# Kernel tuning notes

Measured on AMD Instinct MI355X. Metric: run time of the kernel, lower is better.

Reference implementation:

```python
import jax, jax.numpy as jnp
import numpy as np

INPUT_SIZE = 3072
CORE_SIZE = 1024
OUTPUT_SIZE = 100
BATCH = 8192


def _ri(key, shape, lo, hi):
    # small-range int8 values (torch rand*scale cast to int8)
    return jax.random.randint(key, shape, lo, hi, dtype=jnp.int32).astype(jnp.int8)


def setup_inputs() -> dict:
    key = jax.random.key(0)
    ks = jax.random.split(key, 14)
    return {
        # learned int8 weights (nonzero after EQI.apply updates)
        "W_itoc": _ri(ks[0], (INPUT_SIZE, CORE_SIZE), -3, 4),
        "W_itoc_b": _ri(ks[1], (CORE_SIZE,), -3, 4),
        "W_ctoc": _ri(ks[2], (CORE_SIZE, CORE_SIZE), -3, 4),
        "W_ctoc_b": _ri(ks[3], (CORE_SIZE,), -3, 4),
        "W_ctoo": _ri(ks[4], (CORE_SIZE, OUTPUT_SIZE), -3, 4),
        "W_ctoo_b": _ri(ks[5], (OUTPUT_SIZE,), -3, 4),
        # epsilon perturbations: EPSILON_SCALE=2 -> values in {-1,0,1}
        "e_itoc": _ri(ks[6], (INPUT_SIZE, CORE_SIZE), -2, 2),
        "e_itoc_b": _ri(ks[7], (CORE_SIZE,), -2, 2),
        "e_ctoc": _ri(ks[8], (CORE_SIZE, CORE_SIZE), -2, 2),
        "e_ctoc_b": _ri(ks[9], (CORE_SIZE,), -2, 2),
        "e_ctoo": _ri(ks[10], (CORE_SIZE, OUTPUT_SIZE), -2, 2),
        "e_ctoo_b": _ri(ks[11], (OUTPUT_SIZE,), -2, 2),
        # forward activations
        "inputs": _ri(ks[12], (BATCH, INPUT_SIZE), -4, 5),
        "hiddens": _ri(ks[13], (BATCH, CORE_SIZE), -4, 5),
    }


def _addmm_i8(x, w, b):
    # int8 addmm with wraparound semantics: accumulate in int32, cast back
    # to int8 (truncation == mod-256, matching torch int8 arithmetic).
    acc = jnp.matmul(x.astype(jnp.int32), w.astype(jnp.int32)) + b.astype(jnp.int32)
    return acc.astype(jnp.int8)


def reference(W_itoc, W_itoc_b, W_ctoc, W_ctoc_b, W_ctoo, W_ctoo_b,
              e_itoc, e_itoc_b, e_ctoc, e_ctoc_b, e_ctoo, e_ctoo_b,
              inputs, hiddens):
    # layer 1: inputs -> core (weight = W + epsilon, elementwise int8 add)
    i2c = _addmm_i8(inputs, W_itoc + e_itoc, W_itoc_b + e_itoc_b)      # [B, CORE]
    # layer 2: (hiddens + projected inputs) -> core
    h2 = _addmm_i8(hiddens + i2c, W_ctoc + e_ctoc, W_ctoc_b + e_ctoc_b)  # [B, CORE]
    # layer 3: core -> output
    out = _addmm_i8(h2, W_ctoo + e_ctoo, W_ctoo_b + e_ctoo_b)          # [B, OUT]
    return (h2, out)
```

## Files before the change

### kernel.cpp

```cpp
#include <hip/hip_runtime.h>

typedef int v4i  __attribute__((ext_vector_type(4)));
typedef int v16i __attribute__((ext_vector_type(16)));

__device__ __forceinline__ int pack4i(int a, int b, int c, int d) {
  return (a & 255) | ((b & 255) << 8) | ((c & 255) << 16) | ((d & 255) << 24);
}
__device__ __forceinline__ int badd4(int a, int b) {
  return ((a & 0x7f7f7f7f) + (b & 0x7f7f7f7f)) ^ ((a ^ b) & 0x80808080);
}

__device__ void pack_tile(const int* __restrict__ W, const int* __restrict__ E,
                          char* __restrict__ Bt, int K, int N,
                          int nx, int ky, char* lin) {
  const int t = threadIdx.x;
  const int n0 = nx * 64, k0 = ky * 256;
  {
    const int c  = t & 15;
    const int kq = t >> 4;
    const int ng = n0 + c * 4;
    #pragma unroll 4
    for (int s = 0; s < 16; ++s) {
      const int k = s * 16 + kq;
      const long grow = (long)(k0 + k) * N;
      int a0, a1, a2, a3;
      if (ng + 3 < N) {
        int4 wv = *(const int4*)(W + grow + ng);
        int4 ev = *(const int4*)(E + grow + ng);
        a0 = wv.x + ev.x; a1 = wv.y + ev.y; a2 = wv.z + ev.z; a3 = wv.w + ev.w;
      } else {
        a0 = (ng + 0 < N) ? W[grow + ng + 0] + E[grow + ng + 0] : 0;
        a1 = (ng + 1 < N) ? W[grow + ng + 1] + E[grow + ng + 1] : 0;
        a2 = (ng + 2 < N) ? W[grow + ng + 2] + E[grow + ng + 2] : 0;
        a3 = (ng + 3 < N) ? W[grow + ng + 3] + E[grow + ng + 3] : 0;
      }
      *(int*)(lin + k * 68 + c * 4) = pack4i(a0, a1, a2, a3);
    }
  }
  __syncthreads();
  {
    const int n = t & 63, kq = t >> 6;
    char* dst = Bt + (long)(n0 + n) * K + k0 + (kq << 6);
    int outv[16];
    #pragma unroll
    for (int g = 0; g < 16; ++g) {
      const int k = (kq << 6) + (g << 2);
      outv[g] = pack4i(lin[(k + 0) * 68 + n], lin[(k + 1) * 68 + n],
                       lin[(k + 2) * 68 + n], lin[(k + 3) * 68 + n]);
    }
    #pragma unroll
    for (int g = 0; g < 4; ++g)
      *(int4*)(dst + (g << 4)) =
          make_int4(outv[g * 4], outv[g * 4 + 1], outv[g * 4 + 2], outv[g * 4 + 3]);
  }
}

__global__ __launch_bounds__(256) void pack_weights_kernel(
    const int* W1, const int* E1, char* Bt1,
    const int* W2, const int* E2, char* Bt2,
    const int* W3, const int* E3, char* Bt3,
    const int* b1, const int* eb1, int* bs1,
    const int* b2, const int* eb2, int* bs2,
    const int* b3, const int* eb3, int* bs3) {
  __shared__ __align__(16) char smem[17408];
  const int bid = blockIdx.x;
  if (bid < 192) {
    pack_tile(W1, E1, Bt1, 3072, 1024, bid % 16, bid / 16, smem);
  } else if (bid < 256) {
    const int l = bid - 192;
    pack_tile(W2, E2, Bt2, 1024, 1024, l % 16, l / 16, smem);
  } else if (bid < 264) {
    const int l = bid - 256;
    pack_tile(W3, E3, Bt3, 1024, 100, l & 1, l >> 1, smem);
  } else {
    const int t = threadIdx.x;
    for (int i = t; i < 1024; i += 256) {
      bs1[i] = b1[i] + eb1[i];
      bs2[i] = b2[i] + eb2[i];
    }
    for (int i = t; i < 128; i += 256)
      bs3[i] = (i < 100) ? (b3[i] + eb3[i]) : 0;
  }
}

#define MFMA_I8(a, b, c) __builtin_amdgcn_mfma_i32_32x32x32_i8(a, b, c, 0, 0, 0)

__global__ __launch_bounds__(512, 2) void gemm1_kernel(
    const int* __restrict__ X, const char* __restrict__ Btg,
    const int* __restrict__ bsum, const int* __restrict__ H,
    char* __restrict__ A8out) {
  const int K = 3072;
  __shared__ __align__(16) char smem[61440];
  const int t = threadIdx.x;
  const int bid = blockIdx.x;
  const int mt = bid & 63, nt = bid >> 6;
  const long m0 = (long)mt << 7;
  const int n0 = nt << 8;

  const int lane = t & 63, w = t >> 6;
  const int lc = lane & 31, hg = lane >> 5;
  const int wm = w >> 2, wn = w & 3;

  v16i acc[2][2] = {};

  const int arow = t >> 2, aq = t & 3;
  const int* Xrow = X + (m0 + arow) * (long)K + aq * 16;
  const int aoff = arow * 80 + aq * 16;
  const int brow = t >> 1, bh = t & 1;
  const char* Brow = Btg + (long)(n0 + brow) * K + bh * 32;
  const int boff = 10240 + brow * 80 + bh * 32;

  const int aro = (wm * 64 + lc) * 80 + hg * 16;
  const int bro = 10240 + (wn * 64 + lc) * 80 + hg * 16;

  int4 xa0, xa1, xa2, xa3, xb0, xb1;
  int4 ya0, ya1, ya2, ya3, yb0, yb1;

#define G1_LOAD(p0,p1,p2,p3,p4,p5,kt) do {                        \
    const int kb_ = (kt) << 6;                                    \
    const int* p_ = Xrow + kb_;                                   \
    p0 = *(const int4*)(p_);      p1 = *(const int4*)(p_ + 4);    \
    p2 = *(const int4*)(p_ + 8);  p3 = *(const int4*)(p_ + 12);   \
    p4 = *(const int4*)(Brow + kb_);                              \
    p5 = *(const int4*)(Brow + kb_ + 16);                         \
  } while (0)
#define G1_STORE(p0,p1,p2,p3,p4,p5,stage) do {                    \
    char* base_ = smem + (stage) * 30720;                         \
    *(int4*)(base_ + aoff) = make_int4(                           \
        pack4i(p0.x,p0.y,p0.z,p0.w), pack4i(p1.x,p1.y,p1.z,p1.w), \
        pack4i(p2.x,p2.y,p2.z,p2.w), pack4i(p3.x,p3.y,p3.z,p3.w));\
    *(int4*)(base_ + boff)      = p4;                             \
    *(int4*)(base_ + boff + 16) = p5;                             \
  } while (0)

  auto MFMA_STEP = [&](int stage) {
    const char* base = smem + stage * 30720;
    #pragma unroll
    for (int ks = 0; ks < 2; ++ks) {
      v4i a0 = *(const v4i*)(base + aro + ks * 32);
      v4i a1 = *(const v4i*)(base + aro + 32 * 80 + ks * 32);
      v4i b0 = *(const v4i*)(base + bro + ks * 32);
      v4i b1 = *(const v4i*)(base + bro + 32 * 80 + ks * 32);
      acc[0][0] = MFMA_I8(a0, b0, acc[0][0]);
      acc[0][1] = MFMA_I8(a0, b1, acc[0][1]);
      acc[1][0] = MFMA_I8(a1, b0, acc[1][0]);
      acc[1][1] = MFMA_I8(a1, b1, acc[1][1]);
    }
  };

  const int KIT = K >> 6;
  G1_LOAD(xa0, xa1, xa2, xa3, xb0, xb1, 0);
  G1_LOAD(ya0, ya1, ya2, ya3, yb0, yb1, 1);
  G1_STORE(xa0, xa1, xa2, xa3, xb0, xb1, 0);
  __syncthreads();

  for (int kt = 0; kt < KIT; kt += 2) {
    if (kt + 2 < KIT) G1_LOAD(xa0, xa1, xa2, xa3, xb0, xb1, kt + 2);
    MFMA_STEP(0);
    G1_STORE(ya0, ya1, ya2, ya3, yb0, yb1, 1);
    __syncthreads();
    if (kt + 3 < KIT) G1_LOAD(ya0, ya1, ya2, ya3, yb0, yb1, kt + 3);
    MFMA_STEP(1);
    if (kt + 2 < KIT) {
      G1_STORE(xa0, xa1, xa2, xa3, xb0, xb1, 0);
      __syncthreads();
    }
  }

  __syncthreads();
  const int bsj0 = bsum[n0 + wn * 64 + lc];
  const int bsj1 = bsum[n0 + wn * 64 + 32 + lc];
  #pragma unroll
  for (int i = 0; i < 2; ++i) {
    #pragma unroll
    for (int j = 0; j < 2; ++j) {
      const int bsv = j ? bsj1 : bsj0;
      const int col = wn * 64 + j * 32 + lc;
      #pragma unroll
      for (int r = 0; r < 16; ++r) {
        const int row = wm * 64 + i * 32 + (hg << 2) + (r & 3) + ((r >> 2) << 3);
        smem[row * 272 + col] = (char)(acc[i][j][r] + bsv);
      }
    }
  }
  __syncthreads();
  const int erow = t >> 2, seg = t & 3;
  const char* src = smem + erow * 272 + seg * 64;
  const long gm = m0 + erow;
  const long gco = gm * 1024 + n0 + seg * 64;
  const int* hp = H + gco;
  #pragma unroll
  for (int g = 0; g < 4; ++g) {
    int4 s  = *(const int4*)(src + g * 16);
    int4 h0 = *(const int4*)(hp + g * 16);
    int4 h1 = *(const int4*)(hp + g * 16 + 4);
    int4 h2 = *(const int4*)(hp + g * 16 + 8);
    int4 h3 = *(const int4*)(hp + g * 16 + 12);
    s = make_int4(badd4(s.x, pack4i(h0.x, h0.y, h0.z, h0.w)),
                  badd4(s.y, pack4i(h1.x, h1.y, h1.z, h1.w)),
                  badd4(s.z, pack4i(h2.x, h2.y, h2.z, h2.w)),
                  badd4(s.w, pack4i(h3.x, h3.y, h3.z, h3.w)));
    *(int4*)(A8out + gco + g * 16) = s;
  }
}

__global__ __launch_bounds__(512, 2) void gemm2_kernel(
    const char* __restrict__ A, const char* __restrict__ Btg,
    const int* __restrict__ bsum, int* __restrict__ Iout) {
  const int K = 1024;
  __shared__ __align__(16) char smem[61440];
  const int t = threadIdx.x;
  const int bid = blockIdx.x;
  const int mt = bid & 63, nt = bid >> 6;
  const long m0 = (long)mt << 7;
  const int n0 = nt << 8;

  const int lane = t & 63, w = t >> 6;
  const int lc = lane & 31, hg = lane >> 5;
  const int wm = w >> 2, wn = w & 3;

  v16i acc[2][2] = {};

  const int arow = t >> 2, aq = t & 3;
  const char* Arow = A + (m0 + arow) * (long)K + aq * 16;
  const int aoff = arow * 80 + aq * 16;
  const int brow = t >> 1, bh = t & 1;
  const char* Brow = Btg + (long)(n0 + brow) * K + bh * 32;
  const int boff = 10240 + brow * 80 + bh * 32;

  const int aro = (wm * 64 + lc) * 80 + hg * 16;
  const int bro = 10240 + (wn * 64 + lc) * 80 + hg * 16;

  int4 xa0, xb0, xb1;
  int4 ya0, yb0, yb1;

#define G2_LOAD(p0,p4,p5,kt) do {                                 \
    const int kb_ = (kt) << 6;                                    \
    p0 = *(const int4*)(Arow + kb_);                              \
    p4 = *(const int4*)(Brow + kb_);                              \
    p5 = *(const int4*)(Brow + kb_ + 16);                         \
  } while (0)
#define G2_STORE(p0,p4,p5,stage) do {                             \
    char* base_ = smem + (stage) * 30720;                         \
    *(int4*)(base_ + aoff)      = p0;                             \
    *(int4*)(base_ + boff)      = p4;                             \
    *(int4*)(base_ + boff + 16) = p5;                             \
  } while (0)

  auto MFMA_STEP = [&](int stage) {
    const char* base = smem + stage * 30720;
    #pragma unroll
    for (int ks = 0; ks < 2; ++ks) {
      v4i a0 = *(const v4i*)(base + aro + ks * 32);
      v4i a1 = *(const v4i*)(base + aro + 32 * 80 + ks * 32);
      v4i b0 = *(const v4i*)(base + bro + ks * 32);
      v4i b1 = *(const v4i*)(base + bro + 32 * 80 + ks * 32);
      acc[0][0] = MFMA_I8(a0, b0, acc[0][0]);
      acc[0][1] = MFMA_I8(a0, b1, acc[0][1]);
      acc[1][0] = MFMA_I8(a1, b0, acc[1][0]);
      acc[1][1] = MFMA_I8(a1, b1, acc[1][1]);
    }
  };

  const int KIT = K >> 6;
  G2_LOAD(xa0, xb0, xb1, 0);
  G2_LOAD(ya0, yb0, yb1, 1);
  G2_STORE(xa0, xb0, xb1, 0);
  __syncthreads();

  for (int kt = 0; kt < KIT; kt += 2) {
    if (kt + 2 < KIT) G2_LOAD(xa0, xb0, xb1, kt + 2);
    MFMA_STEP(0);
    G2_STORE(ya0, yb0, yb1, 1);
    __syncthreads();
    if (kt + 3 < KIT) G2_LOAD(ya0, yb0, yb1, kt + 3);
    MFMA_STEP(1);
    if (kt + 2 < KIT) {
      G2_STORE(xa0, xb0, xb1, 0);
      __syncthreads();
    }
  }

  const int bsj0 = bsum[n0 + wn * 64 + lc];
  const int bsj1 = bsum[n0 + wn * 64 + 32 + lc];
  #pragma unroll
  for (int i = 0; i < 2; ++i) {
    #pragma unroll
    for (int j = 0; j < 2; ++j) {
      const int bsv = j ? bsj1 : bsj0;
      const int col = n0 + wn * 64 + j * 32 + lc;
      #pragma unroll
      for (int r = 0; r < 16; ++r) {
        const long row = m0 + wm * 64 + i * 32 + (hg << 2) + (r & 3) + ((r >> 2) << 3);
        Iout[row * 1024 + col] = (int)(signed char)(acc[i][j][r] + bsv);
      }
    }
  }
}

__global__ __launch_bounds__(256, 2) void gemm3_kernel(
    const int* __restrict__ h2, const char* __restrict__ Btg,
    const int* __restrict__ bsum, int* __restrict__ Iout) {
  __shared__ __align__(16) char smem[23040];
  const int t = threadIdx.x;
  const int m0 = blockIdx.x << 4;
  const int lane = t & 63, w = t >> 6;
  const int l16 = lane & 15, q = lane >> 4;
  v4i acc0 = {}, acc1 = {};

  const int am = t >> 4, ah = t & 15;
  const int* Arow = h2 + (long)(m0 + am) * 1024 + ah * 4;
  const int aoff = am * 80 + ah * 4;
  const int bm = t >> 1, bh = t & 1;
  const char* Brow = Btg + (long)bm * 1024 + bh * 32;
  const int boff = bm * 80 + bh * 32;

  const int abo  = l16 * 80 + q * 16;
  const int bbo0 = (w * 32 + l16) * 80 + q * 16;
  const int bbo1 = (w * 32 + 16 + l16) * 80 + q * 16;

  int4 ar, br0, br1;
  auto LOAD = [&](int kt) {
    const int kb = kt << 6;
    ar  = *(const int4*)(Arow + kb);
    br0 = *(const int4*)(Brow + kb);
    br1 = *(const int4*)(Brow + kb + 16);
  };
  auto STORE = [&](int stage) {
    char* base = smem + stage * 11520;
    *(int*)(base + aoff) = pack4i(ar.x, ar.y, ar.z, ar.w);
    *(int4*)(base + 1280 + boff)      = br0;
    *(int4*)(base + 1280 + boff + 16) = br1;
  };
  auto MFMA = [&](int stage) {
    const char* base = smem + stage * 11520;
    v4i a  = *(const v4i*)(base + abo);
    v4i b0 = *(const v4i*)(base + 1280 + bbo0);
    v4i b1 = *(const v4i*)(base + 1280 + bbo1);
    acc0 = __builtin_amdgcn_mfma_i32_16x16x64_i8(a, b0, acc0, 0, 0, 0);
    acc1 = __builtin_amdgcn_mfma_i32_16x16x64_i8(a, b1, acc1, 0, 0, 0);
  };

  LOAD(0); STORE(0); __syncthreads();
  for (int kt = 0; kt < 16; ++kt) {
    if (kt + 1 < 16) LOAD(kt + 1);
    MFMA(kt & 1);
    if (kt + 1 < 16) { STORE((kt + 1) & 1); __syncthreads(); }
  }

  const int c0 = w * 32 + l16;
  const int c1 = c0 + 16;
  if (c0 < 100) {
    const int b = bsum[c0];
    #pragma unroll
    for (int r = 0; r < 4; ++r)
      Iout[(long)(m0 + q * 4 + r) * 100 + c0] = (int)(signed char)(acc0[r] + b);
  }
  if (c1 < 100) {
    const int b = bsum[c1];
    #pragma unroll
    for (int r = 0; r < 4; ++r)
      Iout[(long)(m0 + q * 4 + r) * 100 + c1] = (int)(signed char)(acc1[r] + b);
  }
}

extern "C" void kernel_launch(void* const* d_in, const int* in_sizes, int n_in,
                              void* d_out, int out_size, void* d_ws, size_t ws_size,
                              hipStream_t stream) {
  (void)in_sizes; (void)n_in; (void)out_size; (void)ws_size;
  const int* W1  = (const int*)d_in[0];
  const int* b1  = (const int*)d_in[1];
  const int* W2  = (const int*)d_in[2];
  const int* b2  = (const int*)d_in[3];
  const int* W3  = (const int*)d_in[4];
  const int* b3  = (const int*)d_in[5];
  const int* E1  = (const int*)d_in[6];
  const int* eb1 = (const int*)d_in[7];
  const int* E2  = (const int*)d_in[8];
  const int* eb2 = (const int*)d_in[9];
  const int* E3  = (const int*)d_in[10];
  const int* eb3 = (const int*)d_in[11];
  const int* X   = (const int*)d_in[12];
  const int* H   = (const int*)d_in[13];
  int* out = (int*)d_out;

  char* ws  = (char*)d_ws;
  char* Bt1 = ws;
  char* Bt2 = Bt1 + 3145728;
  char* Bt3 = Bt2 + 1048576;
  int*  bs1 = (int*)(Bt3 + 131072);
  int*  bs2 = bs1 + 1024;
  int*  bs3 = bs2 + 1024;
  char* A2  = (char*)(bs3 + 128);

  pack_weights_kernel<<<dim3(265), dim3(256), 0, stream>>>(
      W1, E1, Bt1, W2, E2, Bt2, W3, E3, Bt3,
      b1, eb1, bs1, b2, eb2, bs2, b3, eb3, bs3);

  gemm1_kernel<<<dim3(256), dim3(512), 0, stream>>>(X, Bt1, bs1, H, A2);

  gemm2_kernel<<<dim3(256), dim3(512), 0, stream>>>(A2, Bt2, bs2, out);

  gemm3_kernel<<<dim3(512), dim3(256), 0, stream>>>(
      out, Bt3, bs3, out + 8388608);
}
```

Baseline: 310.6 us.

## Use async global-to-LDS loads with triple-buffered swizzled tiles in GEMM1/GEMM2

Rewrites the two big int8 GEMMs to use 128x128 tiles with 256 threads, doubling the grid. B (and A in gemm2) tiles move via direct global-to-LDS async loads into an XOR-swizzled, unpadded layout with a three-stage ring, and explicit vmcnt waits replace full syncs. MFMA blocks run at raised wave priority. The aim is to cut register staging, LDS bank conflicts and barrier stalls, at the cost of smaller tiles with less reuse per block and fragile hand-managed wait counts.

```diff
diff --git a/kernel.cpp b/kernel.cpp
--- a/kernel.cpp
+++ b/kernel.cpp
@@ -9,6 +9,17 @@
 __device__ __forceinline__ int badd4(int a, int b) {
   return ((a & 0x7f7f7f7f) + (b & 0x7f7f7f7f)) ^ ((a ^ b) & 0x80808080);
 }
+
+__device__ __forceinline__ void async_ld16(const void* g, void* l) {
+  __builtin_amdgcn_global_load_lds(
+      (const __attribute__((address_space(1))) void*)g,
+      (__attribute__((address_space(3))) void*)l, 16, 0, 0);
+}
+
+#define MFMA_I8(a, b, c) __builtin_amdgcn_mfma_i32_32x32x32_i8(a, b, c, 0, 0, 0)
+#define WAITV(N) asm volatile("s_waitcnt vmcnt(" #N ")" ::: "memory")
+#define BARX do { asm volatile("s_waitcnt lgkmcnt(0)" ::: "memory"); \
+                  __builtin_amdgcn_s_barrier(); } while (0)
 
 __device__ void pack_tile(const int* __restrict__ W, const int* __restrict__ E,
                           char* __restrict__ Bt, int K, int N,
@@ -83,115 +94,139 @@
   }
 }
 
-#define MFMA_I8(a, b, c) __builtin_amdgcn_mfma_i32_32x32x32_i8(a, b, c, 0, 0, 0)
-
-__global__ __launch_bounds__(512, 2) void gemm1_kernel(
+__global__ __launch_bounds__(256, 2) void gemm1_kernel(
     const int* __restrict__ X, const char* __restrict__ Btg,
     const int* __restrict__ bsum, const int* __restrict__ H,
     char* __restrict__ A8out) {
-  const int K = 3072;
-  __shared__ __align__(16) char smem[61440];
+  constexpr int K = 3072, KIT = 48;
+  __shared__ __align__(16) char smem[49152];
   const int t = threadIdx.x;
   const int bid = blockIdx.x;
   const int mt = bid & 63, nt = bid >> 6;
   const long m0 = (long)mt << 7;
-  const int n0 = nt << 8;
+  const int n0 = nt << 7;
 
   const int lane = t & 63, w = t >> 6;
   const int lc = lane & 31, hg = lane >> 5;
-  const int wm = w >> 2, wn = w & 3;
+  const int wm = w >> 1, wn = w & 1;
 
   v16i acc[2][2] = {};
 
-  const int arow = t >> 2, aq = t & 3;
-  const int* Xrow = X + (m0 + arow) * (long)K + aq * 16;
-  const int aoff = arow * 80 + aq * 16;
-  const int brow = t >> 1, bh = t & 1;
-  const char* Brow = Btg + (long)(n0 + brow) * K + bh * 32;
-  const int boff = 10240 + brow * 80 + bh * 32;
-
-  const int aro = (wm * 64 + lc) * 80 + hg * 16;
-  const int bro = 10240 + (wn * 64 + lc) * 80 + hg * 16;
-
-  int4 xa0, xa1, xa2, xa3, xb0, xb1;
-  int4 ya0, ya1, ya2, ya3, yb0, yb1;
-
-#define G1_LOAD(p0,p1,p2,p3,p4,p5,kt) do {                        \
-    const int kb_ = (kt) << 6;                                    \
-    const int* p_ = Xrow + kb_;                                   \
-    p0 = *(const int4*)(p_);      p1 = *(const int4*)(p_ + 4);    \
-    p2 = *(const int4*)(p_ + 8);  p3 = *(const int4*)(p_ + 12);   \
-    p4 = *(const int4*)(Brow + kb_);                              \
-    p5 = *(const int4*)(Brow + kb_ + 16);                         \
-  } while (0)
-#define G1_STORE(p0,p1,p2,p3,p4,p5,stage) do {                    \
-    char* base_ = smem + (stage) * 30720;                         \
-    *(int4*)(base_ + aoff) = make_int4(                           \
-        pack4i(p0.x,p0.y,p0.z,p0.w), pack4i(p1.x,p1.y,p1.z,p1.w), \
-        pack4i(p2.x,p2.y,p2.z,p2.w), pack4i(p3.x,p3.y,p3.z,p3.w));\
-    *(int4*)(base_ + boff)      = p4;                             \
-    *(int4*)(base_ + boff + 16) = p5;                             \
-  } while (0)
-
-  auto MFMA_STEP = [&](int stage) {
-    const char* base = smem + stage * 30720;
-    #pragma unroll
-    for (int ks = 0; ks < 2; ++ks) {
-      v4i a0 = *(const v4i*)(base + aro + ks * 32);
-      v4i a1 = *(const v4i*)(base + aro + 32 * 80 + ks * 32);
-      v4i b0 = *(const v4i*)(base + bro + ks * 32);
-      v4i b1 = *(const v4i*)(base + bro + 32 * 80 + ks * 32);
+  const int arow = t >> 1, ahalf = t & 1;
+  const int* Xrow = X + (m0 + arow) * (long)K + ahalf * 32;
+  const int abase = arow * 64;
+  const int asw0 = ((ahalf * 2 + 0) ^ (arow & 3)) * 16;
+  const int asw1 = ((ahalf * 2 + 1) ^ (arow & 3)) * 16;
+
+  const int brow = w * 32 + (lane >> 2);
+  const int bchunk = ((lane & 3) ^ ((lane >> 2) & 3)) * 16;
+  const char* Bsrc = Btg + (long)(n0 + brow) * K + bchunk;
+
+  const int fa_row = wm * 64 + lc;
+  const int fb_row = wn * 64 + lc;
+  const int sel0 = ((0 * 2 + hg) ^ (lc & 3)) * 16;
+  const int sel1 = ((1 * 2 + hg) ^ (lc & 3)) * 16;
+
+  int4 pX[8], pY[8];
+
+  auto A_ISSUE = [&](int4 (&P)[8], int kt) {
+    const int* p_ = Xrow + kt * 64;
+    #pragma unroll
+    for (int i = 0; i < 8; ++i) P[i] = *(const int4*)(p_ + i * 4);
+  };
+  auto B_ISSUE = [&](int kt, int st) {
+    const char* g_ = Bsrc + (long)kt * 64;
+    char* l_ = smem + st * 16384 + 8192 + w * 2048;
+    async_ld16(g_, l_);
+    async_ld16(g_ + 16 * (long)K, l_ + 1024);
+  };
+  auto A_WRITE = [&](int4 (&P)[8], int st) {
+    char* l_ = smem + st * 16384 + abase;
+    *(int4*)(l_ + asw0) = make_int4(
+        pack4i(P[0].x, P[0].y, P[0].z, P[0].w),
+        pack4i(P[1].x, P[1].y, P[1].z, P[1].w),
+        pack4i(P[2].x, P[2].y, P[2].z, P[2].w),
+        pack4i(P[3].x, P[3].y, P[3].z, P[3].w));
+    *(int4*)(l_ + asw1) = make_int4(
+        pack4i(P[4].x, P[4].y, P[4].z, P[4].w),
+        pack4i(P[5].x, P[5].y, P[5].z, P[5].w),
+        pack4i(P[6].x, P[6].y, P[6].z, P[6].w),
+        pack4i(P[7].x, P[7].y, P[7].z, P[7].w));
+  };
+  auto MSTEP = [&](int st) {
+    const char* ab = smem + st * 16384;
+    const char* bb = ab + 8192;
+    __builtin_amdgcn_s_setprio(1);
+    {
+      v4i a0 = *(const v4i*)(ab + fa_row * 64 + sel0);
+      v4i a1 = *(const v4i*)(ab + (fa_row + 32) * 64 + sel0);
+      v4i b0 = *(const v4i*)(bb + fb_row * 64 + sel0);
+      v4i b1 = *(const v4i*)(bb + (fb_row + 32) * 64 + sel0);
       acc[0][0] = MFMA_I8(a0, b0, acc[0][0]);
       acc[0][1] = MFMA_I8(a0, b1, acc[0][1]);
       acc[1][0] = MFMA_I8(a1, b0, acc[1][0]);
       acc[1][1] = MFMA_I8(a1, b1, acc[1][1]);
     }
-  };
-
-  const int KIT = K >> 6;
-  G1_LOAD(xa0, xa1, xa2, xa3, xb0, xb1, 0);
-  G1_LOAD(ya0, ya1, ya2, ya3, yb0, yb1, 1);
-  G1_STORE(xa0, xa1, xa2, xa3, xb0, xb1, 0);
-  __syncthreads();
-
-  for (int kt = 0; kt < KIT; kt += 2) {
-    if (kt + 2 < KIT) G1_LOAD(xa0, xa1, xa2, xa3, xb0, xb1, kt + 2);
-    MFMA_STEP(0);
-    G1_STORE(ya0, ya1, ya2, ya3, yb0, yb1, 1);
-    __syncthreads();
-    if (kt + 3 < KIT) G1_LOAD(ya0, ya1, ya2, ya3, yb0, yb1, kt + 3);
-    MFMA_STEP(1);
-    if (kt + 2 < KIT) {
-      G1_STORE(xa0, xa1, xa2, xa3, xb0, xb1, 0);
-      __syncthreads();
-    }
-  }
-
-  __syncthreads();
-  const int bsj0 = bsum[n0 + wn * 64 + lc];
-  const int bsj1 = bsum[n0 + wn * 64 + 32 + lc];
+    {
+      v4i a0 = *(const v4i*)(ab + fa_row * 64 + sel1);
+      v4i a1 = *(const v4i*)(ab + (fa_row + 32) * 64 + sel1);
+      v4i b0 = *(const v4i*)(bb + fb_row * 64 + sel1);
+      v4i b1 = *(const v4i*)(bb + (fb_row + 32) * 64 + sel1);
+      acc[0][0] = MFMA_I8(a0, b0, acc[0][0]);
+      acc[0][1] = MFMA_I8(a0, b1, acc[0][1]);
+      acc[1][0] = MFMA_I8(a1, b0, acc[1][0]);
+      acc[1][1] = MFMA_I8(a1, b1, acc[1][1]);
+    }
+    __builtin_amdgcn_s_setprio(0);
+  };
+
+  A_ISSUE(pX, 0); B_ISSUE(0, 0);
+  A_ISSUE(pY, 1); B_ISSUE(1, 1);
+  WAITV(10);
+  A_WRITE(pX, 0);
+  BARX;
+
+  for (int kt = 0; kt < KIT - 2; kt += 2) {
+    A_ISSUE(pX, kt + 2); B_ISSUE(kt + 2, (kt + 2) % 3);
+    MSTEP(kt % 3);
+    WAITV(10);
+    A_WRITE(pY, (kt + 1) % 3);
+    BARX;
+    A_ISSUE(pY, kt + 3); B_ISSUE(kt + 3, (kt + 3) % 3);
+    MSTEP((kt + 1) % 3);
+    WAITV(10);
+    A_WRITE(pX, (kt + 2) % 3);
+    BARX;
+  }
+  MSTEP((KIT - 2) % 3);
+  WAITV(0);
+  A_WRITE(pY, (KIT - 1) % 3);
+  BARX;
+  MSTEP((KIT - 1) % 3);
+
+  BARX;
+  const int bsv0 = bsum[n0 + wn * 64 + lc];
+  const int bsv1 = bsum[n0 + wn * 64 + 32 + lc];
   #pragma unroll
   for (int i = 0; i < 2; ++i) {
     #pragma unroll
     for (int j = 0; j < 2; ++j) {
-      const int bsv = j ? bsj1 : bsj0;
+      const int bv = j ? bsv1 : bsv0;
       const int col = wn * 64 + j * 32 + lc;
       #pragma unroll
       for (int r = 0; r < 16; ++r) {
         const int row = wm * 64 + i * 32 + (hg << 2) + (r & 3) + ((r >> 2) << 3);
-        smem[row * 272 + col] = (char)(acc[i][j][r] + bsv);
+        smem[row * 136 + col] = (char)(acc[i][j][r] + bv);
       }
     }
   }
-  __syncthreads();
-  const int erow = t >> 2, seg = t & 3;
-  const char* src = smem + erow * 272 + seg * 64;
-  const long gm = m0 + erow;
-  const long gco = gm * 1024 + n0 + seg * 64;
+  BARX;
+  const char* srcp = smem + (t >> 1) * 136 + (t & 1) * 64;
+  const long gco = (m0 + (t >> 1)) * 1024 + n0 + (t & 1) * 64;
   const int* hp = H + gco;
   #pragma unroll
   for (int g = 0; g < 4; ++g) {
-    int4 s  = *(const int4*)(src + g * 16);
+    int4 s  = *(const int4*)(srcp + g * 16);
     int4 h0 = *(const int4*)(hp + g * 16);
     int4 h1 = *(const int4*)(hp + g * 16 + 4);
     int4 h2 = *(const int4*)(hp + g * 16 + 8);
@@ -204,82 +239,84 @@
   }
 }
 
-__global__ __launch_bounds__(512, 2) void gemm2_kernel(
+__global__ __launch_bounds__(256, 2) void gemm2_kernel(
     const char* __restrict__ A, const char* __restrict__ Btg,
     const int* __restrict__ bsum, int* __restrict__ Iout) {
-  const int K = 1024;
-  __shared__ __align__(16) char smem[61440];
+  constexpr int K = 1024, KIT = 16;
+  __shared__ __align__(16) char smem[49152];
   const int t = threadIdx.x;
   const int bid = blockIdx.x;
   const int mt = bid & 63, nt = bid >> 6;
   const long m0 = (long)mt << 7;
-  const int n0 = nt << 8;
+  const int n0 = nt << 7;
 
   const int lane = t & 63, w = t >> 6;
   const int lc = lane & 31, hg = lane >> 5;
-  const int wm = w >> 2, wn = w & 3;
+  const int wm = w >> 1, wn = w & 1;
 
   v16i acc[2][2] = {};
 
-  const int arow = t >> 2, aq = t & 3;
-  const char* Arow = A + (m0 + arow) * (long)K + aq * 16;
-  const int aoff = arow * 80 + aq * 16;
-  const int brow = t >> 1, bh = t & 1;
-  const char* Brow = Btg + (long)(n0 + brow) * K + bh * 32;
-  const int boff = 10240 + brow * 80 + bh * 32;
-
-  const int aro = (wm * 64 + lc) * 80 + hg * 16;
-  const int bro = 10240 + (wn * 64 + lc) * 80 + hg * 16;
-
-  int4 xa0, xb0, xb1;
-  int4 ya0, yb0, yb1;
-
-#define G2_LOAD(p0,p4,p5,kt) do {                                 \
-    const int kb_ = (kt) << 6;                                    \
-    p0 = *(const int4*)(Arow + kb_);                              \
-    p4 = *(const int4*)(Brow + kb_);                              \
-    p5 = *(const int4*)(Brow + kb_ + 16);                         \
-  } while (0)
-#define G2_STORE(p0,p4,p5,stage) do {                             \
-    char* base_ = smem + (stage) * 30720;                         \
-    *(int4*)(base_ + aoff)      = p0;                             \
-    *(int4*)(base_ + boff)      = p4;                             \
-    *(int4*)(base_ + boff + 16) = p5;                             \
-  } while (0)
-
-  auto MFMA_STEP = [&](int stage) {
-    const char* base = smem + stage * 30720;
-    #pragma unroll
-    for (int ks = 0; ks < 2; ++ks) {
-      v4i a0 = *(const v4i*)(base + aro + ks * 32);
-      v4i a1 = *(const v4i*)(base + aro + 32 * 80 + ks * 32);
-      v4i b0 = *(const v4i*)(base + bro + ks * 32);
-      v4i b1 = *(const v4i*)(base + bro + 32 * 80 + ks * 32);
+  const int drow = w * 32 + (lane >> 2);
+  const int dchunk = ((lane & 3) ^ ((lane >> 2) & 3)) * 16;
+  const char* Asrc = A   + (m0 + drow) * (long)K + dchunk;
+  const char* Bsrc = Btg + (long)(n0 + drow) * K + dchunk;
+
+  const int fa_row = wm * 64 + lc;
+  const int fb_row = wn * 64 + lc;
+  const int sel0 = ((0 * 2 + hg) ^ (lc & 3)) * 16;
+  const int sel1 = ((1 * 2 + hg) ^ (lc & 3)) * 16;
+
+  auto ISSUE = [&](int kt, int st) {
+    const char* ga = Asrc + (long)kt * 64;
+    const char* gb = Bsrc + (long)kt * 64;
+    char* la = smem + st * 16384 + w * 2048;
+    char* lb = la + 8192;
+    async_ld16(ga, la);
+    async_ld16(ga + 16 * (long)K, la + 1024);
+    async_ld16(gb, lb);
+    async_ld16(gb + 16 * (long)K, lb + 1024);
+  };
+  auto MSTEP = [&](int st) {
+    const char* ab = smem + st * 16384;
+    const char* bb = ab + 8192;
+    __builtin_amdgcn_s_setprio(1);
+    {
+      v4i a0 = *(const v4i*)(ab + fa_row * 64 + sel0);
+      v4i a1 = *(const v4i*)(ab + (fa_row + 32) * 64 + sel0);
+      v4i b0 = *(const v4i*)(bb + fb_row * 64 + sel0);
+      v4i b1 = *(const v4i*)(bb + (fb_row + 32) * 64 + sel0);
       acc[0][0] = MFMA_I8(a0, b0, acc[0][0]);
       acc[0][1] = MFMA_I8(a0, b1, acc[0][1]);
       acc[1][0] = MFMA_I8(a1, b0, acc[1][0]);
       acc[1][1] = MFMA_I8(a1, b1, acc[1][1]);
     }
-  };
-
-  const int KIT = K >> 6;
-  G2_LOAD(xa0, xb0, xb1, 0);
-  G2_LOAD(ya0, yb0, yb1, 1);
-  G2_STORE(xa0, xb0, xb1, 0);
-  __syncthreads();
-
-  for (int kt = 0; kt < KIT; kt += 2) {
-    if (kt + 2 < KIT) G2_LOAD(xa0, xb0, xb1, kt + 2);
-    MFMA_STEP(0);
-    G2_STORE(ya0, yb0, yb1, 1);
-    __syncthreads();
-    if (kt + 3 < KIT) G2_LOAD(ya0, yb0, yb1, kt + 3);
-    MFMA_STEP(1);
-    if (kt + 2 < KIT) {
-      G2_STORE(xa0, xb0, xb1, 0);
-      __syncthreads();
-    }
-  }
+    {
+      v4i a0 = *(const v4i*)(ab + fa_row * 64 + sel1);
+      v4i a1 = *(const v4i*)(ab + (fa_row + 32) * 64 + sel1);
+      v4i b0 = *(const v4i*)(bb + fb_row * 64 + sel1);
+      v4i b1 = *(const v4i*)(bb + (fb_row + 32) * 64 + sel1);
+      acc[0][0] = MFMA_I8(a0, b0, acc[0][0]);
+      acc[0][1] = MFMA_I8(a0, b1, acc[0][1]);
+      acc[1][0] = MFMA_I8(a1, b0, acc[1][0]);
+      acc[1][1] = MFMA_I8(a1, b1, acc[1][1]);
+    }
+    __builtin_amdgcn_s_setprio(0);
+  };
+
+  ISSUE(0, 0);
+  ISSUE(1, 1);
+  WAITV(4);
+  BARX;
+  for (int kt = 0; kt < KIT - 2; ++kt) {
+    ISSUE(kt + 2, (kt + 2) % 3);
+    MSTEP(kt % 3);
+    WAITV(4);
+    BARX;
+  }
+  MSTEP((KIT - 2) % 3);
+  WAITV(0);
+  BARX;
+  MSTEP((KIT - 1) % 3);
 
   const int bsj0 = bsum[n0 + wn * 64 + lc];
   const int bsj1 = bsum[n0 + wn * 64 + 32 + lc];
@@ -287,12 +324,12 @@
   for (int i = 0; i < 2; ++i) {
     #pragma unroll
     for (int j = 0; j < 2; ++j) {
-      const int bsv = j ? bsj1 : bsj0;
+      const int bv = j ? bsj1 : bsj0;
       const int col = n0 + wn * 64 + j * 32 + lc;
       #pragma unroll
       for (int r = 0; r < 16; ++r) {
         const long row = m0 + wm * 64 + i * 32 + (hg << 2) + (r & 3) + ((r >> 2) << 3);
-        Iout[row * 1024 + col] = (int)(signed char)(acc[i][j][r] + bsv);
+        Iout[row * 1024 + col] = (int)(signed char)(acc[i][j][r] + bv);
       }
     }
   }
@@ -397,9 +434,9 @@
       W1, E1, Bt1, W2, E2, Bt2, W3, E3, Bt3,
       b1, eb1, bs1, b2, eb2, bs2, b3, eb3, bs3);
 
-  gemm1_kernel<<<dim3(256), dim3(512), 0, stream>>>(X, Bt1, bs1, H, A2);
-
-  gemm2_kernel<<<dim3(256), dim3(512), 0, stream>>>(A2, Bt2, bs2, out);
+  gemm1_kernel<<<dim3(512), dim3(256), 0, stream>>>(X, Bt1, bs1, H, A2);
+
+  gemm2_kernel<<<dim3(512), dim3(256), 0, stream>>>(A2, Bt2, bs2, out);
 
   gemm3_kernel<<<dim3(512), dim3(256), 0, stream>>>(
       out, Bt3, bs3, out + 8388608);
```

After: 355.1 us. +14.4%, slower.
